# Kernel tuning notes

Measured on AMD Instinct MI355X. Metric: run time of the kernel, lower is better.

## Reference

```python
import jax, jax.numpy as jnp
import numpy as np

N = 100000
E = 1600000
NEG_SLOPE = 0.2
DEPTH = 5


def setup_inputs() -> dict:
    key = jax.random.key(0)
    ks = jax.random.split(key, 8)
    x = jax.random.normal(ks[0], (N, 100), dtype=jnp.float32)
    edge_index = jax.random.randint(ks[1], (2, E), 0, N, dtype=jnp.int64)
    # layer 0: 100 -> 48; layers 1..4: 48 -> 48
    W0 = jax.random.normal(ks[2], (100, 48), dtype=jnp.float32) * 0.1
    Wrest = jax.random.normal(ks[3], (DEPTH - 1, 48, 48), dtype=jnp.float32) * 0.1
    a_src = jax.random.normal(ks[4], (DEPTH, 48), dtype=jnp.float32) * 0.1
    a_dst = jax.random.normal(ks[5], (DEPTH, 48), dtype=jnp.float32) * 0.1
    bias = jax.random.normal(ks[6], (DEPTH, 48), dtype=jnp.float32) * 0.1
    return {"x": x, "edge_index": edge_index, "W0": W0, "Wrest": Wrest,
            "a_src": a_src, "a_dst": a_dst, "bias": bias}


def _gat_layer(x, src, dst, W, a_s, a_d, b):
    h = x @ W                                   # [N, F]
    alpha_s = h @ a_s                           # [N]
    alpha_d = h @ a_d                           # [N]
    e = alpha_s[src] + alpha_d[dst]             # [E']
    e = jax.nn.leaky_relu(e, NEG_SLOPE)
    # segment softmax over edges grouped by destination node
    m = jax.ops.segment_max(e, dst, num_segments=N)
    m = jnp.where(jnp.isfinite(m), m, 0.0)      # empty segments -> 0
    p = jnp.exp(e - m[dst])
    s = jax.ops.segment_sum(p, dst, num_segments=N)
    alpha = p / jnp.maximum(s[dst], 1e-16)      # [E']
    out = jax.ops.segment_sum(alpha[:, None] * h[src], dst, num_segments=N)
    return out + b


def reference(x, edge_index, W0, Wrest, a_src, a_dst, bias):
    # PyG GATConv default add_self_loops=True
    loops = jnp.arange(N, dtype=edge_index.dtype)
    src = jnp.concatenate([edge_index[0], loops])
    dst = jnp.concatenate([edge_index[1], loops])
    Ws = [W0] + [Wrest[i] for i in range(DEPTH - 1)]
    h = x
    for l in range(DEPTH):
        h = _gat_layer(h, src, dst, Ws[l], a_src[l], a_dst[l], bias[l])
        h = jax.nn.elu(h)
    return h
```

## Files before the change

kernel.cpp:

```cpp
#include <hip/hip_runtime.h>

#define NN 100000
#define EE 1600000
#define ETOT (EE + NN)
#define FF 48
#define NEG 0.2f
#define BSH 9
#define BNODES 512
#define NBUK ((NN + BNODES - 1) / BNODES)
#define TILE 2048


__global__ __launch_bounds__(256) void k_bhist(const int* __restrict__ ei,
                                               int* __restrict__ bcnt) {
    __shared__ int h[256];
    int t = threadIdx.x;
    h[t] = 0;
    __syncthreads();
    for (int i = blockIdx.x * 256 + t; i < ETOT; i += gridDim.x * 256) {
        int dd = (i < EE) ? ei[EE + i] : (i - EE);
        atomicAdd(&h[dd >> BSH], 1);
    }
    __syncthreads();
    if (h[t] > 0) atomicAdd(&bcnt[t], h[t]);
}

__global__ void k_bscan(const int* __restrict__ bcnt, int* __restrict__ boff,
                        int* __restrict__ bcur) {
    __shared__ int sb[256];
    int t = threadIdx.x;
    int v = (t < NBUK) ? bcnt[t] : 0;
    sb[t] = v;
    __syncthreads();
    for (int o = 1; o < 256; o <<= 1) {
        int x = (t >= o) ? sb[t - o] : 0;
        __syncthreads();
        sb[t] += x;
        __syncthreads();
    }
    int excl = sb[t] - v;
    boff[t] = excl;
    bcur[t] = excl;
}

__global__ __launch_bounds__(256) void k_bscatter(const int* __restrict__ ei,
                                                  int* __restrict__ bcur,
                                                  int2* __restrict__ pairs) {
    __shared__ int hist[256], incl[256], exc[256], curv[256], gb[256];
    __shared__ int2 stage[TILE];
    __shared__ int staddr[TILE];
    int t = threadIdx.x;
    hist[t] = 0;
    __syncthreads();
    int base = blockIdx.x * TILE;
    int s[8], d[8], b[8];
#pragma unroll
    for (int j = 0; j < 8; j++) {
        int i = base + t + j * 256;
        if (i < ETOT) {
            int ss, dd;
            if (i < EE) { ss = ei[i]; dd = ei[EE + i]; }
            else { ss = i - EE; dd = ss; }
            s[j] = ss; d[j] = dd; b[j] = dd >> BSH;
            atomicAdd(&hist[b[j]], 1);
        } else {
            b[j] = -1;
        }
    }
    __syncthreads();
    int hv = hist[t];
    incl[t] = hv;
    __syncthreads();
    for (int o = 1; o < 256; o <<= 1) {
        int x = (t >= o) ? incl[t - o] : 0;
        __syncthreads();
        incl[t] += x;
        __syncthreads();
    }
    int excl = incl[t] - hv;
    exc[t] = excl;
    curv[t] = excl;
    if (hv > 0) gb[t] = atomicAdd(&bcur[t], hv);
    __syncthreads();
    int total = incl[255];
#pragma unroll
    for (int j = 0; j < 8; j++) {
        if (b[j] >= 0) {
            int pos = atomicAdd(&curv[b[j]], 1);
            stage[pos] = make_int2(s[j], d[j]);
            staddr[pos] = gb[b[j]] + (pos - exc[b[j]]);
        }
    }
    __syncthreads();
    for (int i = t; i < total; i += 256) pairs[staddr[i]] = stage[i];
}

__global__ __launch_bounds__(256) void k_bfill(const int2* __restrict__ pairs,
                                               const int* __restrict__ boff,
                                               int* __restrict__ off,
                                               int* __restrict__ ssrc) {
    __shared__ int cnt[BNODES], cu[BNODES], sb[256];
    int blk = blockIdx.x;
    int t = threadIdx.x;
    int n0 = blk << BSH;
    int beg = boff[blk], end = boff[blk + 1];
    cnt[t] = 0;
    cnt[t + 256] = 0;
    __syncthreads();
    for (int i = beg + t; i < end; i += 256) {
        atomicAdd(&cnt[pairs[i].y - n0], 1);
    }
    __syncthreads();
    int c0 = cnt[2 * t], c1 = cnt[2 * t + 1];
    sb[t] = c0 + c1;
    __syncthreads();
    for (int o = 1; o < 256; o <<= 1) {
        int x = (t >= o) ? sb[t - o] : 0;
        __syncthreads();
        sb[t] += x;
        __syncthreads();
    }
    int e2 = sb[t] - (c0 + c1);
    cu[2 * t] = e2;
    cu[2 * t + 1] = e2 + c0;
    int n1 = min(n0 + BNODES, NN);
    if (n0 + 2 * t < n1) off[n0 + 2 * t] = beg + e2;
    if (n0 + 2 * t + 1 < n1) off[n0 + 2 * t + 1] = beg + e2 + c0;
    if (blk == 0 && t == 0) off[NN] = ETOT;
    __syncthreads();
    for (int i = beg + t; i < end; i += 256) {
        int2 pr = pairs[i];
        int pos = atomicAdd(&cu[pr.y - n0], 1);
        ssrc[beg + pos] = pr.x;
    }
}

template <int K, int KC, int R>
__global__ __launch_bounds__(256) void k_gemm(const float* __restrict__ in,
                                              const float* __restrict__ W,
                                              const float* __restrict__ a_s,
                                              const float* __restrict__ a_d,
                                              float* __restrict__ h,
                                              float* __restrict__ as_,
                                              float* __restrict__ ad_) {
    __shared__ float Wl[K * FF];
    __shared__ float asl[FF], adl[FF];
    int t = threadIdx.x;
    for (int i = t; i < K * FF / 4; i += 256)
        ((float4*)Wl)[i] = ((const float4*)W)[i];
    if (t < FF) { asl[t] = a_s[t]; adl[t] = a_d[t]; }
    __syncthreads();

    int fg = t & 3;
    int pr = t >> 2;
    int r0 = blockIdx.x * (64 * R) + pr * R;
    if (r0 >= NN) return;

    constexpr int NC = K / KC;
    constexpr int QC = KC / 4;
    const float4* x4 = (const float4*)in;
    const float4* wl4 = (const float4*)Wl;

    float acc[R][12];
#pragma unroll
    for (int r = 0; r < R; r++)
#pragma unroll
        for (int j = 0; j < 12; j++) acc[r][j] = 0.f;

    for (int c = 0; c < NC; c++) {
        float xs[R][KC];
#pragma unroll
        for (int r = 0; r < R; r++) {
#pragma unroll
            for (int q = 0; q < QC; q++) {
                float4 v = x4[(size_t)(r0 + r) * (K / 4) + c * QC + q];
                xs[r][4 * q + 0] = v.x; xs[r][4 * q + 1] = v.y;
                xs[r][4 * q + 2] = v.z; xs[r][4 * q + 3] = v.w;
            }
        }
#pragma unroll
        for (int kk = 0; kk < KC; kk++) {
            const int k = c * KC + kk;
            const float4 w0 = wl4[k * 12 + fg * 3 + 0];
            const float4 w1 = wl4[k * 12 + fg * 3 + 1];
            const float4 w2 = wl4[k * 12 + fg * 3 + 2];
#pragma unroll
            for (int r = 0; r < R; r++) {
                const float xv = xs[r][kk];
                acc[r][0] = fmaf(xv, w0.x, acc[r][0]);
                acc[r][1] = fmaf(xv, w0.y, acc[r][1]);
                acc[r][2] = fmaf(xv, w0.z, acc[r][2]);
                acc[r][3] = fmaf(xv, w0.w, acc[r][3]);
                acc[r][4] = fmaf(xv, w1.x, acc[r][4]);
                acc[r][5] = fmaf(xv, w1.y, acc[r][5]);
                acc[r][6] = fmaf(xv, w1.z, acc[r][6]);
                acc[r][7] = fmaf(xv, w1.w, acc[r][7]);
                acc[r][8] = fmaf(xv, w2.x, acc[r][8]);
                acc[r][9] = fmaf(xv, w2.y, acc[r][9]);
                acc[r][10] = fmaf(xv, w2.z, acc[r][10]);
                acc[r][11] = fmaf(xv, w2.w, acc[r][11]);
            }
        }
    }

#pragma unroll
    for (int r = 0; r < R; r++) {
        float4* hp = (float4*)(h + (size_t)(r0 + r) * FF + fg * 12);
        hp[0] = make_float4(acc[r][0], acc[r][1], acc[r][2], acc[r][3]);
        hp[1] = make_float4(acc[r][4], acc[r][5], acc[r][6], acc[r][7]);
        hp[2] = make_float4(acc[r][8], acc[r][9], acc[r][10], acc[r][11]);
    }

    float ps[R], pd[R];
#pragma unroll
    for (int r = 0; r < R; r++) { ps[r] = 0.f; pd[r] = 0.f; }
#pragma unroll
    for (int j = 0; j < 12; j++) {
        float av = asl[fg * 12 + j], dv = adl[fg * 12 + j];
#pragma unroll
        for (int r = 0; r < R; r++) {
            ps[r] = fmaf(acc[r][j], av, ps[r]);
            pd[r] = fmaf(acc[r][j], dv, pd[r]);
        }
    }
#pragma unroll
    for (int r = 0; r < R; r++) {
        ps[r] += __shfl_xor(ps[r], 1); ps[r] += __shfl_xor(ps[r], 2);
        pd[r] += __shfl_xor(pd[r], 1); pd[r] += __shfl_xor(pd[r], 2);
    }
    if (fg == 0) {
#pragma unroll
        for (int r = 0; r < R; r++) {
            as_[r0 + r] = ps[r];
            ad_[r0 + r] = pd[r];
        }
    }
}

__global__ __launch_bounds__(256) void k_aggr(const float* __restrict__ h,
                                              const float* __restrict__ as_,
                                              const float* __restrict__ ad_,
                                              const int* __restrict__ off,
                                              const int* __restrict__ ssrc,
                                              const float* __restrict__ bias,
                                              float* __restrict__ out) {
    int wave = threadIdx.x >> 6;
    int lane = threadIdx.x & 63;
    int d = blockIdx.x * 4 + wave;
    if (d >= NN) return;
    int beg = __builtin_amdgcn_readfirstlane(off[d]);
    int end = __builtin_amdgcn_readfirstlane(off[d + 1]);
    int deg = end - beg;
    float add = ad_[d];
    unsigned foff = (unsigned)((lane < FF ? lane : lane - FF) * 4);
    const char* hb = (const char*)h;

    float acc = 0.f, s = 0.f;

    if (deg <= 64) {
        int srcb = 0;
        float e = -1e30f;
        if (lane < deg) {
            int src = ssrc[beg + lane];
            srcb = src * (FF * 4);
            float t = as_[src] + add;
            e = (t > 0.f) ? t : NEG * t;
        }
        float m = e;
#pragma unroll
        for (int o = 32; o; o >>= 1) m = fmaxf(m, __shfl_xor(m, o));
        float p = (lane < deg) ? __expf(e - m) : 0.f;
        float sv = p;
#pragma unroll
        for (int o = 32; o; o >>= 1) sv += __shfl_xor(sv, o);
        s = sv;

        unsigned pbits = __float_as_uint(p);
        int degR = (deg + 7) & ~7;
        for (int i = 0; i < degR; i += 8) {
            float pj[8], hv[8];
#pragma unroll
            for (int j = 0; j < 8; j++) {
                pj[j] = __uint_as_float(
                    (unsigned)__builtin_amdgcn_readlane((int)pbits, i + j));
                int sbj = __builtin_amdgcn_readlane(srcb, i + j);
                hv[j] = *(const float*)(hb + (unsigned)sbj + foff);
            }
#pragma unroll
            for (int j = 0; j < 8; j++) acc = fmaf(pj[j], hv[j], acc);
        }
    } else {
        int f = lane;
        float m = -1e30f;
        for (int i = beg + lane; i < end; i += 64) {
            float t = as_[ssrc[i]] + add;
            t = (t > 0.f) ? t : NEG * t;
            m = fmaxf(m, t);
        }
#pragma unroll
        for (int o = 32; o; o >>= 1) m = fmaxf(m, __shfl_xor(m, o));
        for (int i = beg; i < end; i++) {
            int src = ssrc[i];
            float e = as_[src] + add;
            e = (e > 0.f) ? e : NEG * e;
            float pp = __expf(e - m);
            s += pp;
            if (f < FF) acc = fmaf(pp, h[(size_t)src * FF + f], acc);
        }
    }

    if (lane < FF) {
        float v = acc / fmaxf(s, 1e-16f) + bias[lane];
        v = (v > 0.f) ? v : (__expf(v) - 1.0f);
        out[(size_t)d * FF + lane] = v;
    }
}


static inline size_t alup(size_t x) { return (x + 255) & ~(size_t)255; }

extern "C" void kernel_launch(void* const* d_in, const int* in_sizes, int n_in,
                              void* d_out, int out_size, void* d_ws, size_t ws_size,
                              hipStream_t stream) {
    const float* x = (const float*)d_in[0];
    const int* ei = (const int*)d_in[1];
    const float* W0 = (const float*)d_in[2];
    const float* Wr = (const float*)d_in[3];
    const float* As = (const float*)d_in[4];
    const float* Ad = (const float*)d_in[5];
    const float* B = (const float*)d_in[6];
    float* out = (float*)d_out;

    char* p = (char*)d_ws;
    int* off = (int*)p;      p += alup((NN + 1) * sizeof(int));
    int* bcnt = (int*)p;     p += alup(256 * sizeof(int));
    int* boff = (int*)p;     p += alup(257 * sizeof(int));
    int* bcur = (int*)p;     p += alup(256 * sizeof(int));
    int2* pairs = (int2*)p;  p += alup((size_t)ETOT * sizeof(int2));
    int* ssrc = (int*)p;     p += alup((size_t)ETOT * sizeof(int) + 256);
    float* htmp = (float*)p; p += alup((size_t)NN * FF * sizeof(float) + 256);
    float* act = (float*)p;  p += alup((size_t)NN * FF * sizeof(float) + 256);
    float* as_ = (float*)p;  p += alup(NN * sizeof(float));
    float* ad_ = (float*)p;  p += alup(NN * sizeof(float));

    hipMemsetAsync(bcnt, 0, 256 * sizeof(int), stream);
    k_bhist<<<512, 256, 0, stream>>>(ei, bcnt);
    k_bscan<<<1, 256, 0, stream>>>(bcnt, boff, bcur);
    k_bscatter<<<(ETOT + TILE - 1) / TILE, 256, 0, stream>>>(ei, bcur, pairs);
    k_bfill<<<NBUK, 256, 0, stream>>>(pairs, boff, off, ssrc);

    for (int l = 0; l < 5; l++) {
        if (l == 0) {
            int g = (NN + 127) / 128;
            k_gemm<100, 20, 2><<<g, 256, 0, stream>>>(x, W0, As, Ad, htmp, as_, ad_);
        } else {
            int g = (NN + 255) / 256;
            k_gemm<48, 16, 4><<<g, 256, 0, stream>>>(act, Wr + (size_t)(l - 1) * 48 * 48,
                                                     As + l * 48, Ad + l * 48, htmp, as_, ad_);
        }
        k_aggr<<<(NN + 3) / 4, 256, 0, stream>>>(htmp, as_, ad_, off, ssrc, B + l * 48,
                                                 (l == 4) ? out : act);
    }
}
```

Baseline: 479.3 us.

## Fuse next layer's 48x48 GEMM and attention projections into aggregation kernel

The aggregation kernel now computes the ELU activation for each destination node and immediately multiplies it by the next layer's weight matrix using wave readlane broadcasts. It also produces the next layer's per-node source/destination attention scalars, so the separate GEMM launches for layers 1-4 and the activation round trip through global memory are removed. Ping-pong buffers hold the layer outputs. In exchange, each wave reads 48x48 weights per node from cache, and inline asm masks the loads to create a false dependency that orders them.

```diff
diff --git a/kernel.cpp b/kernel.cpp
--- a/kernel.cpp
+++ b/kernel.cpp
@@ -134,6 +134,7 @@
         ssrc[beg + pos] = pr.x;
     }
 }
+
 
 template <int K, int KC, int R>
 __global__ __launch_bounds__(256) void k_gemm(const float* __restrict__ in,
@@ -237,13 +238,15 @@
     }
 }
 
-__global__ __launch_bounds__(256) void k_aggr(const float* __restrict__ h,
-                                              const float* __restrict__ as_,
-                                              const float* __restrict__ ad_,
-                                              const int* __restrict__ off,
-                                              const int* __restrict__ ssrc,
-                                              const float* __restrict__ bias,
-                                              float* __restrict__ out) {
+template <bool LAST>
+__global__ __launch_bounds__(256) void k_aggr_fused(
+    const float* __restrict__ h, const float* __restrict__ as_,
+    const float* __restrict__ ad_, const int* __restrict__ off,
+    const int* __restrict__ ssrc, const float* __restrict__ bias_l,
+    const float* __restrict__ Wn, const float* __restrict__ asn,
+    const float* __restrict__ adn, float* __restrict__ hn,
+    float* __restrict__ as_o, float* __restrict__ ad_o,
+    float* __restrict__ out) {
     int wave = threadIdx.x >> 6;
     int lane = threadIdx.x & 63;
     int d = blockIdx.x * 4 + wave;
@@ -252,7 +255,8 @@
     int end = __builtin_amdgcn_readfirstlane(off[d + 1]);
     int deg = end - beg;
     float add = ad_[d];
-    unsigned foff = (unsigned)((lane < FF ? lane : lane - FF) * 4);
+    int fW = (lane < FF) ? lane : lane - FF;
+    unsigned foff = (unsigned)(fW * 4);
     const char* hb = (const char*)h;
 
     float acc = 0.f, s = 0.f;
@@ -290,7 +294,6 @@
             for (int j = 0; j < 8; j++) acc = fmaf(pj[j], hv[j], acc);
         }
     } else {
-        int f = lane;
         float m = -1e30f;
         for (int i = beg + lane; i < end; i += 64) {
             float t = as_[ssrc[i]] + add;
@@ -305,15 +308,60 @@
             e = (e > 0.f) ? e : NEG * e;
             float pp = __expf(e - m);
             s += pp;
-            if (f < FF) acc = fmaf(pp, h[(size_t)src * FF + f], acc);
-        }
-    }
-
-    if (lane < FF) {
-        float v = acc / fmaxf(s, 1e-16f) + bias[lane];
-        v = (v > 0.f) ? v : (__expf(v) - 1.0f);
-        out[(size_t)d * FF + lane] = v;
-    }
+            if (lane < FF) acc = fmaf(pp, h[(size_t)src * FF + lane], acc);
+        }
+    }
+
+    float v = acc / fmaxf(s, 1e-16f) + bias_l[fW];
+    float act = (v > 0.f) ? v : (__expf(v) - 1.0f);
+
+    if (LAST) {
+        if (lane < FF) out[(size_t)d * FF + lane] = act;
+        return;
+    }
+
+    int g0 = __float_as_int(act);
+    asm volatile("v_and_b32 %0, 0, %0" : "+v"(g0));
+    const float* W1 = (const float*)((const char*)Wn + g0);
+
+    float hn_acc = 0.f;
+    {
+        float w[24];
+#pragma unroll
+        for (int k = 0; k < 24; k++) w[k] = W1[k * FF + fW];
+#pragma unroll
+        for (int k = 0; k < 24; k++) {
+            float av = __uint_as_float(
+                (unsigned)__builtin_amdgcn_readlane(__float_as_int(act), k));
+            hn_acc = fmaf(av, w[k], hn_acc);
+        }
+    }
+    int g1 = __float_as_int(hn_acc);
+    asm volatile("v_and_b32 %0, 0, %0" : "+v"(g1));
+    const float* W2 = (const float*)((const char*)Wn + g1);
+    {
+        float w[24];
+#pragma unroll
+        for (int k = 0; k < 24; k++) w[k] = W2[(24 + k) * FF + fW];
+#pragma unroll
+        for (int k = 0; k < 24; k++) {
+            float av = __uint_as_float(
+                (unsigned)__builtin_amdgcn_readlane(__float_as_int(act), 24 + k));
+            hn_acc = fmaf(av, w[k], hn_acc);
+        }
+    }
+
+    float hz = (lane < FF) ? hn_acc : 0.f;
+    float ps = hz * asn[fW];
+    float pd = hz * adn[fW];
+#pragma unroll
+    for (int o = 32; o; o >>= 1) {
+        ps += __shfl_xor(ps, o);
+        pd += __shfl_xor(pd, o);
+    }
+
+    if (lane < FF) hn[(size_t)d * FF + lane] = hn_acc;
+    if (lane == 0) { as_o[d] = ps; ad_o[d] = pd; }
 }
 
 
@@ -338,10 +386,12 @@
     int* bcur = (int*)p;     p += alup(256 * sizeof(int));
     int2* pairs = (int2*)p;  p += alup((size_t)ETOT * sizeof(int2));
     int* ssrc = (int*)p;     p += alup((size_t)ETOT * sizeof(int) + 256);
-    float* htmp = (float*)p; p += alup((size_t)NN * FF * sizeof(float) + 256);
-    float* act = (float*)p;  p += alup((size_t)NN * FF * sizeof(float) + 256);
-    float* as_ = (float*)p;  p += alup(NN * sizeof(float));
-    float* ad_ = (float*)p;  p += alup(NN * sizeof(float));
+    float* hA = (float*)p;   p += alup((size_t)NN * FF * sizeof(float) + 256);
+    float* hB = (float*)p;   p += alup((size_t)NN * FF * sizeof(float) + 256);
+    float* asA = (float*)p;  p += alup(NN * sizeof(float));
+    float* adA = (float*)p;  p += alup(NN * sizeof(float));
+    float* asB = (float*)p;  p += alup(NN * sizeof(float));
+    float* adB = (float*)p;  p += alup(NN * sizeof(float));
 
     hipMemsetAsync(bcnt, 0, 256 * sizeof(int), stream);
     k_bhist<<<512, 256, 0, stream>>>(ei, bcnt);
@@ -349,16 +399,23 @@
     k_bscatter<<<(ETOT + TILE - 1) / TILE, 256, 0, stream>>>(ei, bcur, pairs);
     k_bfill<<<NBUK, 256, 0, stream>>>(pairs, boff, off, ssrc);
 
-    for (int l = 0; l < 5; l++) {
-        if (l == 0) {
-            int g = (NN + 127) / 128;
-            k_gemm<100, 20, 2><<<g, 256, 0, stream>>>(x, W0, As, Ad, htmp, as_, ad_);
-        } else {
-            int g = (NN + 255) / 256;
-            k_gemm<48, 16, 4><<<g, 256, 0, stream>>>(act, Wr + (size_t)(l - 1) * 48 * 48,
-                                                     As + l * 48, Ad + l * 48, htmp, as_, ad_);
-        }
-        k_aggr<<<(NN + 3) / 4, 256, 0, stream>>>(htmp, as_, ad_, off, ssrc, B + l * 48,
-                                                 (l == 4) ? out : act);
-    }
-}
+    int g0 = (NN + 127) / 128;
+    k_gemm<100, 20, 2><<<g0, 256, 0, stream>>>(x, W0, As, Ad, hA, asA, adA);
+
+    int gA = (NN + 3) / 4;
+    k_aggr_fused<false><<<gA, 256, 0, stream>>>(hA, asA, adA, off, ssrc, B + 0,
+                                                Wr + 0 * 2304, As + 48, Ad + 48,
+                                                hB, asB, adB, nullptr);
+    k_aggr_fused<false><<<gA, 256, 0, stream>>>(hB, asB, adB, off, ssrc, B + 48,
+                                                Wr + 1 * 2304, As + 96, Ad + 96,
+                                                hA, asA, adA, nullptr);
+    k_aggr_fused<false><<<gA, 256, 0, stream>>>(hA, asA, adA, off, ssrc, B + 96,
+                                                Wr + 2 * 2304, As + 144, Ad + 144,
+                                                hB, asB, adB, nullptr);
+    k_aggr_fused<false><<<gA, 256, 0, stream>>>(hB, asB, adB, off, ssrc, B + 144,
+                                                Wr + 3 * 2304, As + 192, Ad + 192,
+                                                hA, asA, adA, nullptr);
+    k_aggr_fused<true><<<gA, 256, 0, stream>>>(hA, asA, adA, off, ssrc, B + 192,
+                                               nullptr, nullptr, nullptr,
+                                               nullptr, nullptr, nullptr, out);
+}
```

New measurement: 472.8 us. About the same (-1.4%).

## Fuse layer-0 GEMM with destination bucket histogram; widen bfill blocks to 512

Applied to the files above, without the earlier changes.

The layer-0 feature GEMM and the destination-bucket histogram now run as one launch, with the block index choosing which job a block does, so the two independent jobs overlap and one kernel launch is removed. The GEMM body is moved into a shared device function so the fused kernel and the standalone GEMM can both use it. Separately, the CSR fill kernel uses 512 threads, one per node in the bucket, which makes its scan simpler. In exchange, the shared-memory buffer is sized for the GEMM and histogram blocks also reserve it, which may limit occupancy, and the 512-thread scan needs more barrier steps.

```diff
diff --git a/kernel.cpp b/kernel.cpp
--- a/kernel.cpp
+++ b/kernel.cpp
@@ -9,21 +9,9 @@
 #define BNODES 512
 #define NBUK ((NN + BNODES - 1) / BNODES)
 #define TILE 2048
-
-
-__global__ __launch_bounds__(256) void k_bhist(const int* __restrict__ ei,
-                                               int* __restrict__ bcnt) {
-    __shared__ int h[256];
-    int t = threadIdx.x;
-    h[t] = 0;
-    __syncthreads();
-    for (int i = blockIdx.x * 256 + t; i < ETOT; i += gridDim.x * 256) {
-        int dd = (i < EE) ? ei[EE + i] : (i - EE);
-        atomicAdd(&h[dd >> BSH], 1);
-    }
-    __syncthreads();
-    if (h[t] > 0) atomicAdd(&bcnt[t], h[t]);
-}
+#define G0BLK ((NN + 127) / 128)
+#define HISTBLK 512
+
 
 __global__ void k_bscan(const int* __restrict__ bcnt, int* __restrict__ boff,
                         int* __restrict__ bcur) {
@@ -95,56 +83,52 @@
     for (int i = t; i < total; i += 256) pairs[staddr[i]] = stage[i];
 }
 
-__global__ __launch_bounds__(256) void k_bfill(const int2* __restrict__ pairs,
+__global__ __launch_bounds__(512) void k_bfill(const int2* __restrict__ pairs,
                                                const int* __restrict__ boff,
                                                int* __restrict__ off,
                                                int* __restrict__ ssrc) {
-    __shared__ int cnt[BNODES], cu[BNODES], sb[256];
+    __shared__ int cnt[BNODES], cu[BNODES], sb[512];
     int blk = blockIdx.x;
     int t = threadIdx.x;
     int n0 = blk << BSH;
     int beg = boff[blk], end = boff[blk + 1];
     cnt[t] = 0;
-    cnt[t + 256] = 0;
-    __syncthreads();
-    for (int i = beg + t; i < end; i += 256) {
+    __syncthreads();
+    for (int i = beg + t; i < end; i += 512) {
         atomicAdd(&cnt[pairs[i].y - n0], 1);
     }
     __syncthreads();
-    int c0 = cnt[2 * t], c1 = cnt[2 * t + 1];
-    sb[t] = c0 + c1;
-    __syncthreads();
-    for (int o = 1; o < 256; o <<= 1) {
+    int v = cnt[t];
+    sb[t] = v;
+    __syncthreads();
+    for (int o = 1; o < 512; o <<= 1) {
         int x = (t >= o) ? sb[t - o] : 0;
         __syncthreads();
         sb[t] += x;
         __syncthreads();
     }
-    int e2 = sb[t] - (c0 + c1);
-    cu[2 * t] = e2;
-    cu[2 * t + 1] = e2 + c0;
-    int n1 = min(n0 + BNODES, NN);
-    if (n0 + 2 * t < n1) off[n0 + 2 * t] = beg + e2;
-    if (n0 + 2 * t + 1 < n1) off[n0 + 2 * t + 1] = beg + e2 + c0;
+    int excl = sb[t] - v;
+    cu[t] = excl;
+    if (n0 + t < NN) off[n0 + t] = beg + excl;
     if (blk == 0 && t == 0) off[NN] = ETOT;
     __syncthreads();
-    for (int i = beg + t; i < end; i += 256) {
+    for (int i = beg + t; i < end; i += 512) {
         int2 pr = pairs[i];
         int pos = atomicAdd(&cu[pr.y - n0], 1);
         ssrc[beg + pos] = pr.x;
     }
 }
 
+
 template <int K, int KC, int R>
-__global__ __launch_bounds__(256) void k_gemm(const float* __restrict__ in,
-                                              const float* __restrict__ W,
-                                              const float* __restrict__ a_s,
-                                              const float* __restrict__ a_d,
-                                              float* __restrict__ h,
-                                              float* __restrict__ as_,
-                                              float* __restrict__ ad_) {
-    __shared__ float Wl[K * FF];
-    __shared__ float asl[FF], adl[FF];
+__device__ __forceinline__ void gemm_body(int bid, float* Wl, float* asl, float* adl,
+                                          const float* __restrict__ in,
+                                          const float* __restrict__ W,
+                                          const float* __restrict__ a_s,
+                                          const float* __restrict__ a_d,
+                                          float* __restrict__ h,
+                                          float* __restrict__ as_,
+                                          float* __restrict__ ad_) {
     int t = threadIdx.x;
     for (int i = t; i < K * FF / 4; i += 256)
         ((float4*)Wl)[i] = ((const float4*)W)[i];
@@ -153,7 +137,7 @@
 
     int fg = t & 3;
     int pr = t >> 2;
-    int r0 = blockIdx.x * (64 * R) + pr * R;
+    int r0 = bid * (64 * R) + pr * R;
     if (r0 >= NN) return;
 
     constexpr int NC = K / KC;
@@ -236,6 +220,50 @@
         }
     }
 }
+
+__global__ __launch_bounds__(256) void k_g0_hist(const float* __restrict__ x,
+                                                 const float* __restrict__ W0,
+                                                 const float* __restrict__ a_s,
+                                                 const float* __restrict__ a_d,
+                                                 float* __restrict__ h,
+                                                 float* __restrict__ as_,
+                                                 float* __restrict__ ad_,
+                                                 const int* __restrict__ ei,
+                                                 int* __restrict__ bcnt) {
+    __shared__ __align__(16) char smem[(100 * FF + 2 * FF) * 4];
+    if (blockIdx.x < G0BLK) {
+        float* Wl = (float*)smem;
+        float* asl = Wl + 100 * FF;
+        float* adl = asl + FF;
+        gemm_body<100, 20, 2>(blockIdx.x, Wl, asl, adl, x, W0, a_s, a_d, h, as_, ad_);
+    } else {
+        int* hh = (int*)smem;
+        int t = threadIdx.x;
+        int bid = blockIdx.x - G0BLK;
+        hh[t] = 0;
+        __syncthreads();
+        for (int i = bid * 256 + t; i < ETOT; i += HISTBLK * 256) {
+            int dd = (i < EE) ? ei[EE + i] : (i - EE);
+            atomicAdd(&hh[dd >> BSH], 1);
+        }
+        __syncthreads();
+        if (hh[t] > 0) atomicAdd(&bcnt[t], hh[t]);
+    }
+}
+
+template <int K, int KC, int R>
+__global__ __launch_bounds__(256) void k_gemm(const float* __restrict__ in,
+                                              const float* __restrict__ W,
+                                              const float* __restrict__ a_s,
+                                              const float* __restrict__ a_d,
+                                              float* __restrict__ h,
+                                              float* __restrict__ as_,
+                                              float* __restrict__ ad_) {
+    __shared__ float Wl[K * FF];
+    __shared__ float asl[FF], adl[FF];
+    gemm_body<K, KC, R>(blockIdx.x, Wl, asl, adl, in, W, a_s, a_d, h, as_, ad_);
+}
+
 
 __global__ __launch_bounds__(256) void k_aggr(const float* __restrict__ h,
                                               const float* __restrict__ as_,
@@ -344,16 +372,13 @@
     float* ad_ = (float*)p;  p += alup(NN * sizeof(float));
 
     hipMemsetAsync(bcnt, 0, 256 * sizeof(int), stream);
-    k_bhist<<<512, 256, 0, stream>>>(ei, bcnt);
+    k_g0_hist<<<G0BLK + HISTBLK, 256, 0, stream>>>(x, W0, As, Ad, htmp, as_, ad_, ei, bcnt);
     k_bscan<<<1, 256, 0, stream>>>(bcnt, boff, bcur);
     k_bscatter<<<(ETOT + TILE - 1) / TILE, 256, 0, stream>>>(ei, bcur, pairs);
-    k_bfill<<<NBUK, 256, 0, stream>>>(pairs, boff, off, ssrc);
+    k_bfill<<<NBUK, 512, 0, stream>>>(pairs, boff, off, ssrc);
 
     for (int l = 0; l < 5; l++) {
-        if (l == 0) {
-            int g = (NN + 127) / 128;
-            k_gemm<100, 20, 2><<<g, 256, 0, stream>>>(x, W0, As, Ad, htmp, as_, ad_);
-        } else {
+        if (l > 0) {
             int g = (NN + 255) / 256;
             k_gemm<48, 16, 4><<<g, 256, 0, stream>>>(act, Wr + (size_t)(l - 1) * 48 * 48,
                                                      As + l * 48, Ad + l * 48, htmp, as_, ad_);
```

Measured after the change: 467.8 us. 1.02x faster.
